# Kernel tuning notes

Hardware: AMD Instinct MI355X
Metric: run time of the kernel (lower is better)

## Reference

```python
import jax, jax.numpy as jnp
import numpy as np

BETA = 0.25


def setup_inputs() -> dict:
    key = jax.random.key(0)
    k1, = jax.random.split(key, 1)
    N, D, LEVELS = 1048576, 32, 8
    z_e = jax.random.normal(k1, (N, D), dtype=jnp.float32)
    grid = jnp.linspace(-1.0, 1.0, LEVELS, dtype=jnp.float32)  # FSQ buffer
    return {"z_e": z_e, "grid": grid}


def reference(z_e, grid):
    levels = grid.shape[0]  # static
    z_norm = jnp.tanh(z_e)                                   # [N, D]
    # nearest-level search over the tiny grid (faithful abs-distance argmin)
    dist = jnp.abs(z_norm[:, :, None] - grid[None, None, :])  # [N, D, L]
    indices = jnp.argmin(dist, axis=-1)                       # [N, D] int
    z_q = grid[indices]                                       # [N, D]

    codebook_loss = jnp.mean((z_q - jax.lax.stop_gradient(z_norm)) ** 2)
    commitment_loss = jnp.mean((z_norm - jax.lax.stop_gradient(z_q)) ** 2)
    loss = codebook_loss + BETA * commitment_loss

    # straight-through estimator
    z_q_st = z_norm + jax.lax.stop_gradient(z_q - z_norm)

    # mixed code over first <=4 dims, perplexity = unique fraction
    code_dims = min(indices.shape[1], 4)
    bases = (levels ** jnp.arange(code_dims)).astype(indices.dtype)  # [code_dims]
    mixed_indices = jnp.sum(indices[:, :code_dims] * bases[None, :], axis=1)  # [N]
    n_codes = levels ** code_dims  # static small (4096)
    occupancy = jnp.bincount(mixed_indices, length=n_codes) > 0
    unique_codes = jnp.sum(occupancy).astype(z_e.dtype)
    perplexity = unique_codes / jnp.asarray(float(max(mixed_indices.size, 1)), z_e.dtype)

    return z_q_st, mixed_indices, loss, perplexity
```

## Files before the change

kernel.cpp:

```cpp
#include <hip/hip_runtime.h>
#include <math.h>

#define DD 32

__device__ __forceinline__ int argmin8(float tn, const float g[8]) {
    int bi = 0;
    float bd = fabsf(tn - g[0]);
#pragma unroll
    for (int j = 1; j < 8; ++j) {
        float d = fabsf(tn - g[j]);
        if (d < bd) { bd = d; bi = j; }
    }
    return bi;
}

__global__ __launch_bounds__(256) void fsq_main(
    const float* __restrict__ ze,
    const float* __restrict__ grid,
    float* __restrict__ out,
    int N,
    float* __restrict__ partials,
    int* __restrict__ occ)
{
    float g[8];
#pragma unroll
    for (int j = 0; j < 8; ++j) g[j] = grid[j];

    int t = blockIdx.x * blockDim.x + threadIdx.x;
    float4 w = ((const float4*)ze)[t];
    float xs[4] = {w.x, w.y, w.z, w.w};

    float lsum = 0.f;
    int idx[4];
    float os[4];
#pragma unroll
    for (int e = 0; e < 4; ++e) {
        float x = xs[e];
        float ex = __expf(2.0f * x);
        float tn = 1.0f - 2.0f * __builtin_amdgcn_rcpf(ex + 1.0f);

        float u = (tn + 1.0f) * 3.5f;
        int i0 = (int)rintf(u);
        i0 = min(7, max(0, i0));
        int lo = max(0, i0 - 1), hi = min(7, i0 + 1);
        int bi = lo;
        float bd = fabsf(tn - g[lo]), bd2 = 1e30f;
        for (int j = lo + 1; j <= hi; ++j) {
            float d = fabsf(tn - g[j]);
            if (d < bd) { bd2 = bd; bd = d; bi = j; }
            else if (d < bd2) { bd2 = d; }
        }
        if (bd2 - bd < 1e-5f) {
            tn = (float)tanh((double)x);
            bi = argmin8(tn, g);
        }
        float zq = g[bi];
        float d1 = zq - tn;
        lsum += d1 * d1;
        idx[e] = bi;
        os[e] = tn + d1;
    }
    ((float4*)out)[t] = make_float4(os[0], os[1], os[2], os[3]);

    if ((t & 7) == 0) {
        int row = t >> 3;
        int mixed = idx[0] + 8 * idx[1] + 64 * idx[2] + 512 * idx[3];
        out[(size_t)N * DD + row] = (float)mixed;
        occ[mixed] = 1;
    }

    float s = lsum;
#pragma unroll
    for (int off = 32; off > 0; off >>= 1) s += __shfl_down(s, off);
    __shared__ float sh[4];
    if ((threadIdx.x & 63) == 0) sh[threadIdx.x >> 6] = s;
    __syncthreads();
    if (threadIdx.x == 0) {
        partials[blockIdx.x] = sh[0] + sh[1] + sh[2] + sh[3];
    }
}

__global__ __launch_bounds__(256) void fsq_tail(
    const float* __restrict__ partials, int nblocks,
    const int* __restrict__ occ,
    float* __restrict__ out, int N)
{
    double s = 0.0;
    for (int i = threadIdx.x; i < nblocks; i += 256) s += (double)partials[i];
    int cnt = 0;
    for (int i = threadIdx.x; i < 4096; i += 256) cnt += (occ[i] != 0) ? 1 : 0;
#pragma unroll
    for (int off = 32; off > 0; off >>= 1) {
        s += __shfl_down(s, off);
        cnt += __shfl_down(cnt, off);
    }
    __shared__ double shs[4];
    __shared__ int shc[4];
    if ((threadIdx.x & 63) == 0) { shs[threadIdx.x >> 6] = s; shc[threadIdx.x >> 6] = cnt; }
    __syncthreads();
    if (threadIdx.x == 0) {
        double total = shs[0] + shs[1] + shs[2] + shs[3];
        int unique = shc[0] + shc[1] + shc[2] + shc[3];
        double mean = total / ((double)N * (double)DD);
        size_t base = (size_t)N * DD + (size_t)N;
        out[base] = (float)(1.25 * mean);
        out[base + 1] = (float)unique / (float)N;
    }
}

extern "C" void kernel_launch(void* const* d_in, const int* in_sizes, int n_in,
                              void* d_out, int out_size, void* d_ws, size_t ws_size,
                              hipStream_t stream) {
    const float* ze   = (const float*)d_in[0];
    const float* grid = (const float*)d_in[1];
    float* out = (float*)d_out;
    int N = in_sizes[0] / DD;

    int threads = (N * DD) / 4;
    int block = 256;
    int nblocks = threads / block;

    float* partials = (float*)d_ws;
    int* occ = (int*)((char*)d_ws + (size_t)nblocks * sizeof(float));
    hipMemsetAsync(occ, 0, 4096 * sizeof(int), stream);

    fsq_main<<<nblocks, block, 0, stream>>>(ze, grid, out, N, partials, occ);
    fsq_tail<<<1, 256, 0, stream>>>(partials, nblocks, occ, out, N);
}
```

Baseline: 285.7 us.

## Precompute grid decision thresholds and use a grid-stride persistent main kernel

A setup kernel bisects the float bit patterns to find the exact tie-break threshold between each pair of adjacent grid levels, and it also zeroes the occupancy table in place of the memset. The main kernel then finds the level index by counting how many thresholds tanh(x) exceeds, and it only falls back to double-precision tanh when the value lies near a threshold. The main kernel now runs a fixed 2048-block grid-stride loop, so there are far fewer blocks and fewer partial sums to reduce. The thresholding removes per-element branchy argmin work. It adds a tiny extra kernel launch and depends on the bisection matching the reference's argmin tie behaviour.

Result: faster. 248.9 us (-12.9%).

```diff
diff --git a/kernel.cpp b/kernel.cpp
--- a/kernel.cpp
+++ b/kernel.cpp
@@ -2,71 +2,88 @@
 #include <math.h>
 
 #define DD 32
+#define NB 2048
+#define BS 256
 
-__device__ __forceinline__ int argmin8(float tn, const float g[8]) {
-    int bi = 0;
-    float bd = fabsf(tn - g[0]);
-#pragma unroll
-    for (int j = 1; j < 8; ++j) {
-        float d = fabsf(tn - g[j]);
-        if (d < bd) { bd = d; bi = j; }
+__device__ __forceinline__ unsigned int fkey(float f) {
+    unsigned int u = __float_as_uint(f);
+    return (u & 0x80000000u) ? ~u : (u | 0x80000000u);
+}
+__device__ __forceinline__ float funkey(unsigned int k) {
+    unsigned int u = (k & 0x80000000u) ? (k ^ 0x80000000u) : ~k;
+    return __uint_as_float(u);
+}
+
+__global__ __launch_bounds__(256) void fsq_setup(
+    const float* __restrict__ grid,
+    float* __restrict__ thr,
+    int* __restrict__ occ)
+{
+    int t = threadIdx.x;
+    if (t < 7) {
+        float a = grid[t], b = grid[t + 1];
+        unsigned int lo = fkey(a), hi = fkey(b);
+        while (hi - lo > 1u) {
+            unsigned int mid = lo + (hi - lo) / 2u;
+            float x = funkey(mid);
+            if (fabsf(x - b) < fabsf(x - a)) hi = mid; else lo = mid;
+        }
+        thr[t] = funkey(lo);
     }
-    return bi;
+    int4* o4 = (int4*)occ;
+    for (int i = t; i < 1024; i += 256) o4[i] = make_int4(0, 0, 0, 0);
 }
 
 __global__ __launch_bounds__(256) void fsq_main(
     const float* __restrict__ ze,
     const float* __restrict__ grid,
+    const float* __restrict__ thr,
     float* __restrict__ out,
     int N,
     float* __restrict__ partials,
     int* __restrict__ occ)
 {
-    float g[8];
+    __shared__ float gs[8];
+    if (threadIdx.x < 8) gs[threadIdx.x] = grid[threadIdx.x];
+    float T0 = thr[0], T1 = thr[1], T2 = thr[2], T3 = thr[3];
+    float T4 = thr[4], T5 = thr[5], T6 = thr[6];
+    __syncthreads();
+
+    const int Q = N * DD / 4;
+    const int stride = gridDim.x * blockDim.x;
+    float lsum = 0.f;
+
+    for (int i = blockIdx.x * blockDim.x + threadIdx.x; i < Q; i += stride) {
+        float4 w = ((const float4*)ze)[i];
+        float xs[4] = {w.x, w.y, w.z, w.w};
+        float os[4];
+        int idx[4];
 #pragma unroll
-    for (int j = 0; j < 8; ++j) g[j] = grid[j];
+        for (int e = 0; e < 4; ++e) {
+            float x = xs[e];
+            float ex = __expf(2.0f * x);
+            float tn = 1.0f - 2.0f * __builtin_amdgcn_rcpf(ex + 1.0f);
+            float m = fminf(fminf(fminf(fabsf(tn - T0), fabsf(tn - T1)),
+                                  fminf(fabsf(tn - T2), fabsf(tn - T3))),
+                            fminf(fminf(fabsf(tn - T4), fabsf(tn - T5)),
+                                  fabsf(tn - T6)));
+            if (m < 1e-5f) tn = (float)tanh((double)x);
+            int bi = (tn > T0) + (tn > T1) + (tn > T2) + (tn > T3)
+                   + (tn > T4) + (tn > T5) + (tn > T6);
+            float zq = gs[bi];
+            float d1 = zq - tn;
+            lsum += d1 * d1;
+            os[e] = tn + d1;
+            idx[e] = bi;
+        }
+        ((float4*)out)[i] = make_float4(os[0], os[1], os[2], os[3]);
 
-    int t = blockIdx.x * blockDim.x + threadIdx.x;
-    float4 w = ((const float4*)ze)[t];
-    float xs[4] = {w.x, w.y, w.z, w.w};
-
-    float lsum = 0.f;
-    int idx[4];
-    float os[4];
-#pragma unroll
-    for (int e = 0; e < 4; ++e) {
-        float x = xs[e];
-        float ex = __expf(2.0f * x);
-        float tn = 1.0f - 2.0f * __builtin_amdgcn_rcpf(ex + 1.0f);
-
-        float u = (tn + 1.0f) * 3.5f;
-        int i0 = (int)rintf(u);
-        i0 = min(7, max(0, i0));
-        int lo = max(0, i0 - 1), hi = min(7, i0 + 1);
-        int bi = lo;
-        float bd = fabsf(tn - g[lo]), bd2 = 1e30f;
-        for (int j = lo + 1; j <= hi; ++j) {
-            float d = fabsf(tn - g[j]);
-            if (d < bd) { bd2 = bd; bd = d; bi = j; }
-            else if (d < bd2) { bd2 = d; }
+        if ((i & 7) == 0) {
+            int row = i >> 3;
+            int mixed = idx[0] + 8 * idx[1] + 64 * idx[2] + 512 * idx[3];
+            out[(size_t)N * DD + row] = (float)mixed;
+            occ[mixed] = 1;
         }
-        if (bd2 - bd < 1e-5f) {
-            tn = (float)tanh((double)x);
-            bi = argmin8(tn, g);
-        }
-        float zq = g[bi];
-        float d1 = zq - tn;
-        lsum += d1 * d1;
-        idx[e] = bi;
-        os[e] = tn + d1;
-    }
-    ((float4*)out)[t] = make_float4(os[0], os[1], os[2], os[3]);
-
-    if ((t & 7) == 0) {
-        int row = t >> 3;
-        int mixed = idx[0] + 8 * idx[1] + 64 * idx[2] + 512 * idx[3];
-        out[(size_t)N * DD + row] = (float)mixed;
-        occ[mixed] = 1;
     }
 
     float s = lsum;
@@ -75,9 +92,8 @@
     __shared__ float sh[4];
     if ((threadIdx.x & 63) == 0) sh[threadIdx.x >> 6] = s;
     __syncthreads();
-    if (threadIdx.x == 0) {
+    if (threadIdx.x == 0)
         partials[blockIdx.x] = sh[0] + sh[1] + sh[2] + sh[3];
-    }
 }
 
 __global__ __launch_bounds__(256) void fsq_tail(
@@ -116,14 +132,11 @@
     float* out = (float*)d_out;
     int N = in_sizes[0] / DD;
 
-    int threads = (N * DD) / 4;
-    int block = 256;
-    int nblocks = threads / block;
+    float* partials = (float*)d_ws;
+    int* occ = (int*)((char*)d_ws + 8192);
+    float* thr = (float*)((char*)d_ws + 24576);
 
-    float* partials = (float*)d_ws;
-    int* occ = (int*)((char*)d_ws + (size_t)nblocks * sizeof(float));
-    hipMemsetAsync(occ, 0, 4096 * sizeof(int), stream);
-
-    fsq_main<<<nblocks, block, 0, stream>>>(ze, grid, out, N, partials, occ);
-    fsq_tail<<<1, 256, 0, stream>>>(partials, nblocks, occ, out, N);
+    fsq_setup<<<1, 256, 0, stream>>>(grid, thr, occ);
+    fsq_main<<<NB, BS, 0, stream>>>(ze, grid, thr, out, N, partials, occ);
+    fsq_tail<<<1, 256, 0, stream>>>(partials, NB, occ, out, N);
 }
```
